# Kernel optimization log

Measured on AMD Instinct MI355X. Metric: run time of the kernel, lower is better.

## Reference

```python
import jax, jax.numpy as jnp
import numpy as np

LMAX = 6
F_IN = 512      # sphere_fdim
F_HID = 8       # f_hidden
N_PTS = 192     # s2 healpix grid points (projector & feature-sphere kernel)
N_SO3GRID = 4000  # SO3Activation grid (resolution=10, ~20x10x20)
N_CONVGRID = 192  # so3_near_identity_grid (8 alpha x 3 beta x 8 gamma)
S2_DIM = (LMAX + 1) ** 2                            # 49
SO3_DIM = sum((2 * l + 1) ** 2 for l in range(LMAX + 1))  # 455
B = 128
C_ENC = 2048
H = W = 7


def setup_inputs() -> dict:
    key = jax.random.key(0)
    ks = jax.random.split(key, 11)
    return {
        "fmap": jax.random.normal(ks[0], (B, C_ENC, H, W), jnp.float32),
        "conv_w": jax.random.normal(ks[1], (F_IN, C_ENC), jnp.float32) / np.sqrt(C_ENC).astype(np.float32),
        "conv_b": jnp.zeros((F_IN,), jnp.float32),
        "proj_w": jax.random.uniform(ks[2], (H, W, N_PTS), jnp.float32) / (H * W),
        "proj_Y": jax.random.normal(ks[3], (N_PTS, S2_DIM), jnp.float32),
        "fs_w": jax.random.normal(ks[4], (F_IN, F_HID, N_PTS), jnp.float32),
        "fs_Y": jax.random.normal(ks[5], (N_PTS, S2_DIM), jnp.float32),
        "act_to": jax.random.normal(ks[6], (SO3_DIM, N_SO3GRID), jnp.float32) / np.sqrt(SO3_DIM).astype(np.float32),
        "act_from": jax.random.normal(ks[7], (N_SO3GRID, SO3_DIM), jnp.float32) / np.float32(N_SO3GRID),
        "so3_w": jax.random.normal(ks[8], (F_HID, 1, N_CONVGRID), jnp.float32),
        "so3_D": jax.random.normal(ks[9], (N_CONVGRID, SO3_DIM), jnp.float32),
    }


def _s2_to_so3_linear(x, psi, f_in):
    # e3nn o3.Linear(s2_irreps -> so3_irreps, internal_weights=False).
    # x: (B, f_in, S2_DIM) with per-l blocks of size 2l+1 (mul=1).
    # psi: (f_in, f_out, S2_DIM). Per l: outer product of input irrep with
    # weight irrep -> (2l+1)x(2l+1) Wigner block; path norm 1/sqrt(f_in*mul_in).
    outs = []
    for l in range(LMAX + 1):
        s, e = l * l, (l + 1) ** 2
        xl = x[:, :, s:e]          # (B, f_in, 2l+1)
        wl = psi[:, :, s:e]        # (f_in, f_out, 2l+1)
        ol = jnp.einsum('bfm,fgu->bgum', xl, wl) / np.sqrt(f_in).astype(np.float32)
        outs.append(ol.reshape(ol.shape[0], ol.shape[1], -1))
    return jnp.concatenate(outs, axis=-1)   # (B, f_out, SO3_DIM)


def _so3_to_so3_linear(x, psi, f_in):
    # e3nn o3.Linear(so3_irreps -> so3_irreps, internal_weights=False).
    # x: (B, f_in, SO3_DIM), per-l block (mul=2l+1, dim=2l+1) flattened [u, m].
    # psi: (f_in, f_out, SO3_DIM), per-l block (u_in, u_out).
    outs = []
    off = 0
    for l in range(LMAX + 1):
        d = 2 * l + 1
        xl = x[:, :, off:off + d * d].reshape(x.shape[0], f_in, d, d)
        wl = psi[:, :, off:off + d * d].reshape(f_in, psi.shape[1], d, d)
        ol = jnp.einsum('bfum,fguv->bgvm', xl, wl) / np.sqrt(f_in * d).astype(np.float32)
        outs.append(ol.reshape(ol.shape[0], ol.shape[1], -1))
        off += d * d
    return jnp.concatenate(outs, axis=-1)


def reference(fmap, conv_w, conv_b, proj_w, proj_Y, fs_w, fs_Y, act_to, act_from, so3_w, so3_D):
    # --- SpatialS2Projector: 1x1 conv, orthographic-grid weighting, S2 FT ---
    x = jnp.einsum('bchw,fc->bfhw', fmap, conv_w) + conv_b[None, :, None, None]
    x = jnp.einsum('bfhw,hwn->bfn', x, proj_w)                   # (B, 512, N_PTS)
    x = jnp.einsum('bfn,ni->bfi', x, proj_Y) / np.sqrt(N_PTS).astype(np.float32)  # (B, 512, 49)
    # --- feature sphere -> external weight for o3.Linear (S2 conv theorem) ---
    psi = jnp.einsum('fgn,ni->fgi', fs_w, fs_Y) / np.sqrt(N_PTS).astype(np.float32)  # (512, 8, 49)
    x = _s2_to_so3_linear(x, psi, F_IN)                          # (B, 8, 455)
    # --- SO3Activation: synthesize signal on SO3 grid, relu, analyze back ---
    g = jax.nn.relu(jnp.einsum('bfi,in->bfn', x, act_to))        # (B, 8, N_SO3GRID)
    x = jnp.einsum('bfn,ni->bfi', g, act_from)                   # (B, 8, 455)
    # --- SO3Convolution over near-identity grid ---
    psi2 = jnp.einsum('fgn,ni->fgi', so3_w, so3_D) / np.sqrt(N_CONVGRID).astype(np.float32)  # (8, 1, 455)
    x = _so3_to_so3_linear(x, psi2, F_HID)                       # (B, 1, 455)
    return x
```

## Files before the change

kernel.cpp:

```cpp
#include <hip/hip_runtime.h>
#include <hip/hip_bf16.h>

#define NB    128
#define CENC  2048
#define FIN   512
#define FHID  8
#define S2D   49
#define SO3D  455
#define HW    49

typedef unsigned short ushort_t;
typedef __bf16 bf16x8 __attribute__((ext_vector_type(8)));
typedef float  f32x4  __attribute__((ext_vector_type(4)));

#define GLD16(gp, lp) __builtin_amdgcn_global_load_lds( \
    (__attribute__((address_space(1))) const unsigned int*)(gp), \
    (__attribute__((address_space(3))) unsigned int*)(lp), 16, 0, 0)

__device__ __forceinline__ int soff(int l) { return l*(4*l*l-1)/3; }

__device__ __forceinline__ ushort_t f2bf(float x) {
  __hip_bfloat16 h = __float2bfloat16(x);
  return *reinterpret_cast<ushort_t*>(&h);
}
__device__ __forceinline__ float bf2f(ushort_t u) {
  __hip_bfloat16 h = *reinterpret_cast<__hip_bfloat16*>(&u);
  return __bfloat162float(h);
}


__device__ __forceinline__ void dev_gemm_nn(float* smem,
    const float* __restrict__ A, const float* __restrict__ B, float* __restrict__ C,
    int M, int N, int K, int lda, int ldb, int ldc, float alpha, int bx, int by,
    int cmode, ushort_t* __restrict__ psiTout)
{
  float* As = smem;
  float* Bs = smem + 32*68;
  const int tid = threadIdx.x;
  const int tx = tid & 15, ty = tid >> 4;
  const int n0 = bx * 64, m0 = by * 64;
  float acc[4][4] = {};
  for (int k0 = 0; k0 < K; k0 += 32) {
    {
      const int kk = tid & 31, mmB = tid >> 5;
      #pragma unroll
      for (int j = 0; j < 8; ++j) {
        const int mm = mmB + 8*j;
        const int m = m0 + mm, k = k0 + kk;
        As[kk*68 + mm] = (m < M && k < K) ? A[(size_t)m*lda + k] : 0.f;
      }
    }
    {
      const int nn = tid & 63, kkB = tid >> 6;
      #pragma unroll
      for (int j = 0; j < 8; ++j) {
        const int kk = kkB + 4*j;
        const int n = n0 + nn, k = k0 + kk;
        Bs[kk*68 + nn] = (n < N && k < K) ? B[(size_t)k*ldb + n] : 0.f;
      }
    }
    __syncthreads();
    #pragma unroll
    for (int kk = 0; kk < 32; ++kk) {
      const float4 a4 = *(const float4*)&As[kk*68 + ty*4];
      const float4 b4 = *(const float4*)&Bs[kk*68 + tx*4];
      const float av[4] = {a4.x,a4.y,a4.z,a4.w};
      const float bv[4] = {b4.x,b4.y,b4.z,b4.w};
      #pragma unroll
      for (int i = 0; i < 4; ++i)
        #pragma unroll
        for (int j = 0; j < 4; ++j)
          acc[i][j] = fmaf(av[i], bv[j], acc[i][j]);
    }
    __syncthreads();
  }
  if (cmode == 1) {
    #pragma unroll
    for (int i = 0; i < 4; ++i) {
      const int m = m0 + ty*4 + i;
      const int f = m >> 3, g = m & 7;
      #pragma unroll
      for (int j = 0; j < 4; ++j) {
        const int n = tx*4 + j;
        psiTout[(size_t)(g*64 + n)*512 + f] = (n < 49) ? f2bf(acc[i][j]*alpha) : (ushort_t)0;
      }
    }
    return;
  }
  #pragma unroll
  for (int i = 0; i < 4; ++i) {
    const int m = m0 + ty*4 + i;
    if (m >= M) continue;
    #pragma unroll
    for (int j = 0; j < 4; ++j) {
      const int n = n0 + tx*4 + j;
      if (n >= N) continue;
      C[(size_t)m*ldc + n] = acc[i][j] * alpha;
    }
  }
}

__device__ __forceinline__ void dev_transpose_cvt64(float* smem,
    const float* __restrict__ in, int R, int C,
    ushort_t* __restrict__ out, int Rp, int Cp, int bx, int by)
{
  float (*t)[65] = (float(*)[65])smem;
  const int c0 = bx*64, r0 = by*64;
  const int tid = threadIdx.x;
  const int cl = tid & 63, rlB = tid >> 6;
  #pragma unroll
  for (int p = 0; p < 16; ++p) {
    const int rl = rlB + p*4;
    const int r = r0 + rl, c = c0 + cl;
    t[rl][cl] = (r < R && c < C) ? in[(size_t)r*C + c] : 0.f;
  }
  __syncthreads();
  #pragma unroll
  for (int p = 0; p < 4; ++p) {
    const int c = p*16 + (tid >> 4);
    const int r4 = (tid & 15) * 4;
    unsigned int lo = (unsigned int)f2bf(t[r4+0][c]) | ((unsigned int)f2bf(t[r4+1][c]) << 16);
    unsigned int hi = (unsigned int)f2bf(t[r4+2][c]) | ((unsigned int)f2bf(t[r4+3][c]) << 16);
    *(uint2*)&out[(size_t)(c0 + c)*Rp + r0 + r4] = make_uint2(lo, hi);
  }
}

__device__ __forceinline__ void dev_sumP(float* smem,
    const float* __restrict__ proj_w, const float* __restrict__ proj_Y,
    float* __restrict__ sumP)
{
  float* colsum = smem;
  const int tid = threadIdx.x;
  if (tid < 192) {
    float s = 0.f;
    for (int h = 0; h < 49; ++h) s += proj_w[h*192 + tid];
    colsum[tid] = s;
  }
  __syncthreads();
  if (tid < 64) {
    float s = 0.f;
    if (tid < 49) for (int k = 0; k < 192; ++k) s += colsum[k] * proj_Y[k*49 + tid];
    sumP[tid] = (tid < 49) ? s * 0.07216878364870323f : 0.f;
  }
}

__global__ __launch_bounds__(256) void prep_all(
    const float* __restrict__ conv_w,
    const float* __restrict__ proj_w, const float* __restrict__ proj_Y,
    const float* __restrict__ fs_w, const float* __restrict__ fs_Y,
    const float* __restrict__ act_to, const float* __restrict__ act_from,
    const float* __restrict__ so3_w, const float* __restrict__ so3_D,
    float* __restrict__ wP, float* __restrict__ wSumP, float* __restrict__ wPsi2,
    ushort_t* __restrict__ psiT,
    ushort_t* __restrict__ actToT, ushort_t* __restrict__ actFromT,
    ushort_t* __restrict__ cwT)
{
  __shared__ float smem[4352];
  const int blk = blockIdx.x;
  const float is192 = 0.07216878364870323f;
  if (blk < 1) {
    dev_gemm_nn(smem, proj_w, proj_Y, wP, 49,49,192, 192,49,49, is192, 0, 0, 0, nullptr);
  } else if (blk < 9) {
    dev_gemm_nn(smem, so3_w, so3_D, wPsi2, 8,455,192, 192,455,455, is192, blk-1, 0, 0, nullptr);
  } else if (blk < 73) {
    dev_gemm_nn(smem, fs_w, fs_Y, nullptr, 4096,49,192, 192,49,0, is192, 0, blk-9, 1, psiT);
  } else if (blk < 585) {
    const int t = blk-73;   dev_transpose_cvt64(smem, act_to, 455, 4000, actToT, 512, 4096, t & 63, t >> 6);
  } else if (blk < 1097) {
    const int t = blk-585;  dev_transpose_cvt64(smem, act_from, 4000, 455, actFromT, 4096, 512, t & 7, t >> 3);
  } else if (blk < 1353) {
    const int t = blk-1097; dev_transpose_cvt64(smem, conv_w, 512, 2048, cwT, 512, 2048, t & 31, t >> 5);
  } else {
    dev_sumP(smem, proj_w, proj_Y, wSumP);
  }
}

__global__ __launch_bounds__(256) void xpt_gemm(
    const float* __restrict__ fmap, const float* __restrict__ wP,
    ushort_t* __restrict__ xPT)
{
  __shared__ ushort_t Wl[64*64];
  __shared__ ushort_t Fl[128*64];
  const int tid = threadIdx.x;
  const int b = blockIdx.x >> 4, ct = blockIdx.x & 15;
  const int c0 = ct*128;
  for (int idx = tid; idx < 4096; idx += 256) {
    const int i = idx >> 6, hw = idx & 63;
    const float v = (i < 49 && hw < 49) ? wP[hw*49 + i] : 0.f;
    const int pos = i*64 + ((((hw>>3) ^ (i & 7)) << 3) | (hw & 7));
    Wl[pos] = f2bf(v);
  }
  const float* src = fmap + ((size_t)b*CENC + c0)*HW;
  #pragma unroll
  for (int q = 0; q < 7; ++q) {
    const int f4 = q*256 + tid;
    if (f4 < 1568) {
      const float4 v = *(const float4*)&src[f4*4];
      const float vv[4] = {v.x,v.y,v.z,v.w};
      const int e0 = f4*4;
      #pragma unroll
      for (int t = 0; t < 4; ++t) {
        const int e = e0 + t;
        const int r = e/49, hw = e - r*49;
        const int pos = r*64 + ((((hw>>3) ^ (r & 7)) << 3) | (hw & 7));
        Fl[pos] = f2bf(vv[t]);
      }
    }
  }
  for (int idx = tid; idx < 128*15; idx += 256) {
    const int r = idx/15, hw = 49 + (idx - (idx/15)*15);
    const int pos = r*64 + ((((hw>>3) ^ (r & 7)) << 3) | (hw & 7));
    Fl[pos] = 0;
  }
  __syncthreads();

  const int wv = tid >> 6, ln = tid & 63;
  const int col = ln & 15, quad = ln >> 4;
  f32x4 acc[4][2];
  #pragma unroll
  for (int i = 0; i < 4; ++i)
    #pragma unroll
    for (int j = 0; j < 2; ++j)
      acc[i][j] = (f32x4){0.f,0.f,0.f,0.f};
  #pragma unroll
  for (int ks = 0; ks < 2; ++ks) {
    bf16x8 af[4], bfr[2];
    #pragma unroll
    for (int i = 0; i < 4; ++i) {
      const int row = i*16 + col;
      af[i] = *(bf16x8*)&Wl[row*64 + (((ks*4 + quad) ^ (row & 7)) << 3)];
    }
    #pragma unroll
    for (int j = 0; j < 2; ++j) {
      const int row = wv*32 + j*16 + col;
      bfr[j] = *(bf16x8*)&Fl[row*64 + (((ks*4 + quad) ^ (row & 7)) << 3)];
    }
    #pragma unroll
    for (int i = 0; i < 4; ++i)
      #pragma unroll
      for (int j = 0; j < 2; ++j)
        acc[i][j] = __builtin_amdgcn_mfma_f32_16x16x32_bf16(af[i], bfr[j], acc[i][j], 0, 0, 0);
  }
  #pragma unroll
  for (int i = 0; i < 4; ++i) {
    #pragma unroll
    for (int j = 0; j < 2; ++j) {
      #pragma unroll
      for (int r = 0; r < 4; ++r) {
        const int irow = i*16 + quad*4 + r;
        const int c = c0 + wv*32 + j*16 + col;
        xPT[(size_t)(b*64 + irow)*2048 + c] = f2bf(acc[i][j][r]);
      }
    }
  }
}

__global__ __launch_bounds__(256) void gemm_w2t(
    const ushort_t* __restrict__ A, const ushort_t* __restrict__ B,
    const float* __restrict__ conv_b,
    ushort_t* __restrict__ Cb, float* __restrict__ bpsi)
{
  __shared__ ushort_t Alds[64*64];
  __shared__ ushort_t Blds[128*64];
  __shared__ float bred[256];
  const int tid = threadIdx.x;
  const int wv = tid >> 6, ln = tid & 63;
  const int col = ln & 15, quad = ln >> 4;
  const int m0 = blockIdx.y * 64, n0 = blockIdx.x * 128;
  const int lda = 512, ldb = 512, ldc = 2048, K = 512;
  const bool doB = (blockIdx.x == 0);
  const int br = tid & 63, bp = tid >> 6;

  const int rl = ln >> 3;
  const int gsw = (ln & 7) ^ rl;
  const ushort_t* aP[2]; const ushort_t* bP[4];
  ushort_t* aL[2]; ushort_t* bL[4];
  #pragma unroll
  for (int r = 0; r < 2; ++r) {
    const int R = wv*16 + r*8;
    aP[r] = A + (size_t)(m0 + R + rl)*lda + gsw*8;
    aL[r] = &Alds[R*64];
  }
  #pragma unroll
  for (int r = 0; r < 4; ++r) {
    const int R = wv*32 + r*8;
    bP[r] = B + (size_t)(n0 + R + rl)*ldb + gsw*8;
    bL[r] = &Blds[R*64];
  }

  f32x4 acc[4][2];
  #pragma unroll
  for (int i = 0; i < 4; ++i)
    #pragma unroll
    for (int j = 0; j < 2; ++j)
      acc[i][j] = (f32x4){0.f,0.f,0.f,0.f};
  float bacc = 0.f;

  for (int k0 = 0; k0 < K; k0 += 64) {
    #pragma unroll
    for (int r = 0; r < 2; ++r) { GLD16(aP[r], aL[r]); aP[r] += 64; }
    #pragma unroll
    for (int r = 0; r < 4; ++r) { GLD16(bP[r], bL[r]); bP[r] += 64; }
    __syncthreads();
    #pragma unroll
    for (int ks = 0; ks < 2; ++ks) {
      bf16x8 af[4], bfr[2];
      #pragma unroll
      for (int i = 0; i < 4; ++i) {
        const int row = i*16 + col;
        af[i] = *(bf16x8*)&Alds[row*64 + (((ks*4 + quad) ^ (row & 7)) << 3)];
      }
      #pragma unroll
      for (int j = 0; j < 2; ++j) {
        const int row = wv*32 + j*16 + col;
        bfr[j] = *(bf16x8*)&Blds[row*64 + (((ks*4 + quad) ^ (row & 7)) << 3)];
      }
      #pragma unroll
      for (int i = 0; i < 4; ++i)
        #pragma unroll
        for (int j = 0; j < 2; ++j)
          acc[i][j] = __builtin_amdgcn_mfma_f32_16x16x32_bf16(af[i], bfr[j], acc[i][j], 0, 0, 0);
    }
    if (doB) {
      #pragma unroll
      for (int qq = 0; qq < 2; ++qq) {
        const int q = bp*2 + qq;
        const int lo = (q ^ (br & 7)) << 3;
        #pragma unroll
        for (int e = 0; e < 8; ++e)
          bacc = fmaf(conv_b[k0 + q*8 + e], bf2f(Alds[br*64 + lo + e]), bacc);
      }
    }
    __syncthreads();
  }

  #pragma unroll
  for (int i = 0; i < 4; ++i) {
    const int mBase = m0 + i*16 + quad*4;
    #pragma unroll
    for (int j = 0; j < 2; ++j) {
      const int n = n0 + wv*32 + j*16 + col;
      #pragma unroll
      for (int r = 0; r < 4; ++r)
        Cb[(size_t)(mBase+r)*ldc + n] = f2bf(acc[i][j][r]);
    }
  }
  if (doB) {
    bred[bp*64 + br] = bacc;
    __syncthreads();
    if (tid < 64)
      bpsi[m0 + tid] = bred[tid] + bred[64+tid] + bred[128+tid] + bred[192+tid];
  }
}

__global__ __launch_bounds__(256) void y_blockdiag(
    const ushort_t* __restrict__ xPT, const ushort_t* __restrict__ W2T,
    const float* __restrict__ sumP, const float* __restrict__ bpsi,
    ushort_t* __restrict__ y)
{
  const int blk = blockIdx.x, tid = threadIdx.x;
  if (blk >= 164) {
    const int bz = blk - 164;
    for (int idx = tid; idx < 7296; idx += 256) {
      const int row = bz*128 + idx/57, cp = 455 + (idx - (idx/57)*57);
      y[(size_t)row*512 + cp] = 0;
    }
    return;
  }
  __shared__ ushort_t Asl[64*64];
  __shared__ ushort_t Bsl[64*64];
  int l, lstart;
  if      (blk < 2)   { l=0; lstart=0; }
  else if (blk < 8)   { l=1; lstart=2; }
  else if (blk < 18)  { l=2; lstart=8; }
  else if (blk < 32)  { l=3; lstart=18; }
  else if (blk < 68)  { l=4; lstart=32; }
  else if (blk < 112) { l=5; lstart=68; }
  else                { l=6; lstart=112; }
  const int d = 2*l+1, ll = l*l, Ml = 8*d;
  const int local = blk - lstart, ntc = 2*d;
  const int mt = local / ntc, nt = local - mt*ntc;
  const int m0 = mt*64, n0 = nt*64;

  const int wv = tid >> 6, ln = tid & 63;
  const int col = ln & 15, quad = ln >> 4;
  const int wr = wv >> 1, wc = wv & 1;
  const int rl = ln >> 3;
  const int gsw = (ln & 7) ^ rl;

  const ushort_t* aP[2]; const ushort_t* bP[2];
  ushort_t* aL[2]; ushort_t* bL[2];
  #pragma unroll
  for (int r = 0; r < 2; ++r) {
    const int R = wv*16 + r*8;
    const int mu = m0 + R + rl;
    int grow;
    if (mu < Ml) { const int g = mu/d, u = mu - g*d; grow = g*64 + ll + u; }
    else grow = 511;
    aP[r] = W2T + (size_t)grow*2048 + gsw*8;
    aL[r] = &Asl[R*64];
    const int nu = n0 + R + rl;
    const int bb = nu/d, m = nu - bb*d;
    bP[r] = xPT + (size_t)(bb*64 + ll + m)*2048 + gsw*8;
    bL[r] = &Bsl[R*64];
  }

  f32x4 acc[2][2];
  #pragma unroll
  for (int i = 0; i < 2; ++i)
    #pragma unroll
    for (int j = 0; j < 2; ++j)
      acc[i][j] = (f32x4){0.f,0.f,0.f,0.f};

  for (int k0 = 0; k0 < 2048; k0 += 64) {
    #pragma unroll
    for (int r = 0; r < 2; ++r) { GLD16(aP[r], aL[r]); aP[r] += 64; }
    #pragma unroll
    for (int r = 0; r < 2; ++r) { GLD16(bP[r], bL[r]); bP[r] += 64; }
    __syncthreads();
    #pragma unroll
    for (int ks = 0; ks < 2; ++ks) {
      bf16x8 af[2], bfr[2];
      #pragma unroll
      for (int i = 0; i < 2; ++i) {
        const int row = wr*32 + i*16 + col;
        af[i] = *(bf16x8*)&Asl[row*64 + (((ks*4 + quad) ^ (row & 7)) << 3)];
      }
      #pragma unroll
      for (int j = 0; j < 2; ++j) {
        const int row = wc*32 + j*16 + col;
        bfr[j] = *(bf16x8*)&Bsl[row*64 + (((ks*4 + quad) ^ (row & 7)) << 3)];
      }
      #pragma unroll
      for (int i = 0; i < 2; ++i)
        #pragma unroll
        for (int j = 0; j < 2; ++j)
          acc[i][j] = __builtin_amdgcn_mfma_f32_16x16x32_bf16(af[i], bfr[j], acc[i][j], 0, 0, 0);
    }
    __syncthreads();
  }

  const float isq512 = 0.044194173824159216f;
  const int sol = soff(l);
  #pragma unroll
  for (int i = 0; i < 2; ++i) {
    #pragma unroll
    for (int j = 0; j < 2; ++j) {
      #pragma unroll
      for (int r = 0; r < 4; ++r) {
        const int mu = m0 + wr*32 + i*16 + quad*4 + r;
        if (mu >= Ml) continue;
        const int nu = n0 + wc*32 + j*16 + col;
        const int g = mu/d, u = mu - g*d;
        const int bb = nu/d, m = nu - bb*d;
        const float v = (acc[i][j][r] + sumP[ll+m]*bpsi[g*64 + ll + u]) * isq512;
        y[(size_t)(bb*8 + g)*512 + sol + u*d + m] = f2bf(v);
      }
    }
  }
}

__global__ __launch_bounds__(512) void gemm8w_nt(
    const ushort_t* __restrict__ A, const ushort_t* __restrict__ B, void* __restrict__ Cv,
    int M, int N, int K, int lda, int ldb, int ldc,
    int mode, int kPartLen)
{
  __shared__ ushort_t Alds[128*64];
  __shared__ ushort_t Blds[128*64];
  const int tid = threadIdx.x;
  const int wv = tid >> 6, ln = tid & 63;
  const int col = ln & 15, quad = ln >> 4;
  const int wr = wv >> 2, wc = wv & 3;
  const int m0 = blockIdx.y * 128, n0 = blockIdx.x * 128;
  int kStart = 0, kEnd = K;
  float*    C  = (float*)Cv;
  ushort_t* Cb = (ushort_t*)Cv;
  if (mode == 2) {
    kStart = blockIdx.z * kPartLen;
    kEnd = min(K, kStart + kPartLen);
    C += (size_t)blockIdx.z * (size_t)M * (size_t)ldc;
  }

  const int rl = ln >> 3;
  const int gsw = (ln & 7) ^ rl;
  const ushort_t* aP[2]; const ushort_t* bP[2];
  ushort_t* aL[2]; ushort_t* bL[2];
  #pragma unroll
  for (int r = 0; r < 2; ++r) {
    const int R = wv*16 + r*8;
    aP[r] = A + (size_t)(m0 + R + rl)*lda + kStart + gsw*8;
    aL[r] = &Alds[R*64];
    bP[r] = B + (size_t)(n0 + R + rl)*ldb + kStart + gsw*8;
    bL[r] = &Blds[R*64];
  }

  f32x4 acc[4][2];
  #pragma unroll
  for (int i = 0; i < 4; ++i)
    #pragma unroll
    for (int j = 0; j < 2; ++j)
      acc[i][j] = (f32x4){0.f,0.f,0.f,0.f};

  for (int k0 = kStart; k0 < kEnd; k0 += 64) {
    #pragma unroll
    for (int r = 0; r < 2; ++r) { GLD16(aP[r], aL[r]); aP[r] += 64; }
    #pragma unroll
    for (int r = 0; r < 2; ++r) { GLD16(bP[r], bL[r]); bP[r] += 64; }
    __syncthreads();
    #pragma unroll
    for (int ks = 0; ks < 2; ++ks) {
      bf16x8 af[4], bfr[2];
      #pragma unroll
      for (int i = 0; i < 4; ++i) {
        const int row = wr*64 + i*16 + col;
        af[i] = *(bf16x8*)&Alds[row*64 + (((ks*4 + quad) ^ (row & 7)) << 3)];
      }
      #pragma unroll
      for (int j = 0; j < 2; ++j) {
        const int row = wc*32 + j*16 + col;
        bfr[j] = *(bf16x8*)&Blds[row*64 + (((ks*4 + quad) ^ (row & 7)) << 3)];
      }
      #pragma unroll
      for (int i = 0; i < 4; ++i)
        #pragma unroll
        for (int j = 0; j < 2; ++j)
          acc[i][j] = __builtin_amdgcn_mfma_f32_16x16x32_bf16(af[i], bfr[j], acc[i][j], 0, 0, 0);
    }
    __syncthreads();
  }

  #pragma unroll
  for (int i = 0; i < 4; ++i) {
    const int mBase = m0 + wr*64 + i*16 + quad*4;
    #pragma unroll
    for (int j = 0; j < 2; ++j) {
      const int n = n0 + wc*32 + j*16 + col;
      if (mode == 1) {
        #pragma unroll
        for (int r = 0; r < 4; ++r)
          Cb[(size_t)(mBase+r)*ldc + n] = f2bf(fmaxf(acc[i][j][r], 0.f));
      } else {
        #pragma unroll
        for (int r = 0; r < 4; ++r)
          C[(size_t)(mBase+r)*ldc + n] = acc[i][j][r];
      }
    }
  }
}

__global__ __launch_bounds__(512) void so3_final(
    const float* __restrict__ zpart, const float* __restrict__ psi2,
    float* __restrict__ out)
{
  __shared__ float Zs[8*SO3D];
  __shared__ float P2s[8*SO3D];
  const int b = blockIdx.x, tid = threadIdx.x;
  for (int idx = tid; idx < 8*SO3D; idx += 512) {
    const int f = idx / SO3D, i = idx - f*SO3D;
    float s = 0.f;
    #pragma unroll
    for (int p = 0; p < 8; ++p)
      s += zpart[((size_t)p*1024 + (size_t)b*FHID + f)*512 + i];
    Zs[idx] = s;
    P2s[idx] = psi2[idx];
  }
  __syncthreads();
  if (tid < SO3D) {
    const int i = tid;
    int l;
    if (i < 1) l = 0; else if (i < 10) l = 1; else if (i < 35) l = 2;
    else if (i < 84) l = 3; else if (i < 165) l = 4; else if (i < 286) l = 5; else l = 6;
    const int so = soff(l), d = 2*l+1;
    const int r = i - so;
    const int v = r / d, m = r - v*d;
    float acc = 0.f;
    for (int f = 0; f < 8; ++f)
      for (int u = 0; u < d; ++u)
        acc = fmaf(Zs[f*SO3D + so + u*d + m], P2s[f*SO3D + so + u*d + v], acc);
    const float scale = rsqrtf(8.0f * (float)d);
    out[(size_t)b*SO3D + i] = acc * scale;
  }
}

extern "C" void kernel_launch(void* const* d_in, const int* in_sizes, int n_in,
                              void* d_out, int out_size, void* d_ws, size_t ws_size,
                              hipStream_t stream) {
  const float* fmap    = (const float*)d_in[0];
  const float* conv_w  = (const float*)d_in[1];
  const float* conv_b  = (const float*)d_in[2];
  const float* proj_w  = (const float*)d_in[3];
  const float* proj_Y  = (const float*)d_in[4];
  const float* fs_w    = (const float*)d_in[5];
  const float* fs_Y    = (const float*)d_in[6];
  const float* act_to  = (const float*)d_in[7];
  const float* act_from= (const float*)d_in[8];
  const float* so3_w   = (const float*)d_in[9];
  const float* so3_D   = (const float*)d_in[10];
  float* out           = (float*)d_out;

  char* wsb = (char*)d_ws;
  float*    wP       = (float*)(wsb + 0);
  float*    wSumP    = (float*)(wsb + 9728);
  float*    wPsi2    = (float*)(wsb + 9984);
  ushort_t* actToT   = (ushort_t*)(wsb + 24576);
  ushort_t* actFromT = (ushort_t*)(wsb + 4218880);
  ushort_t* yPad     = (ushort_t*)(wsb + 8413184);
  ushort_t* psiT     = (ushort_t*)(wsb + 9461760);
  float*    bpsi     = (float*)(wsb + 9986048);
  ushort_t* W2T      = (ushort_t*)(wsb + 9988096);
  ushort_t* xPT      = (ushort_t*)(wsb + 12085248);
  ushort_t* cwT      = (ushort_t*)(wsb + 45639680);
  ushort_t* gBuf     = (ushort_t*)(wsb + 12085248);
  float*    zPart    = (float*)(wsb + 20473856);

  prep_all<<<dim3(1354), 256, 0, stream>>>(
      conv_w, proj_w, proj_Y, fs_w, fs_Y, act_to, act_from, so3_w, so3_D,
      wP, wSumP, wPsi2, psiT, actToT, actFromT, cwT);
  xpt_gemm<<<dim3(2048), 256, 0, stream>>>(fmap, wP, xPT);
  gemm_w2t<<<dim3(16,8), 256, 0, stream>>>(psiT, cwT, conv_b, W2T, bpsi);
  y_blockdiag<<<dim3(172), 256, 0, stream>>>(xPT, W2T, wSumP, bpsi, yPad);
  gemm8w_nt<<<dim3(32,8), 512, 0, stream>>>(yPad, actToT, gBuf,
      1024, 4096, 512, 512, 512, 4096, 1, 0);
  gemm8w_nt<<<dim3(4,8,8), 512, 0, stream>>>(gBuf, actFromT, zPart,
      1024, 512, 4096, 4096, 4096, 512, 2, 512);
  so3_final<<<dim3(128), 512, 0, stream>>>(zPart, wPsi2, out);
}
```

Measured before the change: 222.9 us.

## Merge xpt and w2t GEMMs into one launch, precompute swizzled bf16 projection weight

```diff
diff --git a/kernel.cpp b/kernel.cpp
--- a/kernel.cpp
+++ b/kernel.cpp
@@ -32,7 +32,7 @@
 __device__ __forceinline__ void dev_gemm_nn(float* smem,
     const float* __restrict__ A, const float* __restrict__ B, float* __restrict__ C,
     int M, int N, int K, int lda, int ldb, int ldc, float alpha, int bx, int by,
-    int cmode, ushort_t* __restrict__ psiTout)
+    int cmode, ushort_t* __restrict__ uOut)
 {
   float* As = smem;
   float* Bs = smem + 32*68;
@@ -82,7 +82,20 @@
       #pragma unroll
       for (int j = 0; j < 4; ++j) {
         const int n = tx*4 + j;
-        psiTout[(size_t)(g*64 + n)*512 + f] = (n < 49) ? f2bf(acc[i][j]*alpha) : (ushort_t)0;
+        uOut[(size_t)(g*64 + n)*512 + f] = (n < 49) ? f2bf(acc[i][j]*alpha) : (ushort_t)0;
+      }
+    }
+    return;
+  }
+  if (cmode == 2) {
+    #pragma unroll
+    for (int i = 0; i < 4; ++i) {
+      const int m = ty*4 + i;
+      #pragma unroll
+      for (int j = 0; j < 4; ++j) {
+        const int n = tx*4 + j;
+        const float v = (m < 49 && n < 49) ? acc[i][j]*alpha : 0.f;
+        uOut[n*64 + ((((m>>3) ^ (n&7)) << 3) | (m&7))] = f2bf(v);
       }
     }
     return;
@@ -150,7 +163,7 @@
     const float* __restrict__ fs_w, const float* __restrict__ fs_Y,
     const float* __restrict__ act_to, const float* __restrict__ act_from,
     const float* __restrict__ so3_w, const float* __restrict__ so3_D,
-    float* __restrict__ wP, float* __restrict__ wSumP, float* __restrict__ wPsi2,
+    ushort_t* __restrict__ wPT64, float* __restrict__ wSumP, float* __restrict__ wPsi2,
     ushort_t* __restrict__ psiT,
     ushort_t* __restrict__ actToT, ushort_t* __restrict__ actFromT,
     ushort_t* __restrict__ cwT)
@@ -159,7 +172,7 @@
   const int blk = blockIdx.x;
   const float is192 = 0.07216878364870323f;
   if (blk < 1) {
-    dev_gemm_nn(smem, proj_w, proj_Y, wP, 49,49,192, 192,49,49, is192, 0, 0, 0, nullptr);
+    dev_gemm_nn(smem, proj_w, proj_Y, nullptr, 49,49,192, 192,49,0, is192, 0, 0, 2, wPT64);
   } else if (blk < 9) {
     dev_gemm_nn(smem, so3_w, so3_D, wPsi2, 8,455,192, 192,455,455, is192, blk-1, 0, 0, nullptr);
   } else if (blk < 73) {
@@ -175,46 +188,47 @@
   }
 }
 
-__global__ __launch_bounds__(256) void xpt_gemm(
-    const float* __restrict__ fmap, const float* __restrict__ wP,
-    ushort_t* __restrict__ xPT)
-{
-  __shared__ ushort_t Wl[64*64];
-  __shared__ ushort_t Fl[128*64];
+__device__ __forceinline__ void dev_xpt(
+    ushort_t* Wl, ushort_t* Fl,
+    const float* __restrict__ fmap, const ushort_t* __restrict__ wPT64,
+    ushort_t* __restrict__ xPT, int blk)
+{
   const int tid = threadIdx.x;
-  const int b = blockIdx.x >> 4, ct = blockIdx.x & 15;
+  const int wv = tid >> 6, ln = tid & 63;
+  const int b = blk >> 4, ct = blk & 15;
   const int c0 = ct*128;
-  for (int idx = tid; idx < 4096; idx += 256) {
-    const int i = idx >> 6, hw = idx & 63;
-    const float v = (i < 49 && hw < 49) ? wP[hw*49 + i] : 0.f;
-    const int pos = i*64 + ((((hw>>3) ^ (i & 7)) << 3) | (hw & 7));
-    Wl[pos] = f2bf(v);
-  }
+  #pragma unroll
+  for (int q = 0; q < 2; ++q)
+    GLD16(wPT64 + (wv*2+q)*512 + ln*8, Wl + (wv*2+q)*512);
   const float* src = fmap + ((size_t)b*CENC + c0)*HW;
+  int r = (tid*4)/49, hw = tid*4 - r*49;
   #pragma unroll
   for (int q = 0; q < 7; ++q) {
     const int f4 = q*256 + tid;
     if (f4 < 1568) {
-      const float4 v = *(const float4*)&src[f4*4];
-      const float vv[4] = {v.x,v.y,v.z,v.w};
-      const int e0 = f4*4;
+      const float4 v = *(const float4*)&src[(size_t)f4*4];
+      const float vv[4] = {v.x, v.y, v.z, v.w};
+      int rr = r, hh = hw;
       #pragma unroll
       for (int t = 0; t < 4; ++t) {
-        const int e = e0 + t;
-        const int r = e/49, hw = e - r*49;
-        const int pos = r*64 + ((((hw>>3) ^ (r & 7)) << 3) | (hw & 7));
-        Fl[pos] = f2bf(vv[t]);
-      }
-    }
-  }
-  for (int idx = tid; idx < 128*15; idx += 256) {
-    const int r = idx/15, hw = 49 + (idx - (idx/15)*15);
-    const int pos = r*64 + ((((hw>>3) ^ (r & 7)) << 3) | (hw & 7));
-    Fl[pos] = 0;
+        Fl[rr*64 + ((((hh>>3) ^ (rr&7)) << 3) | (hh&7))] = f2bf(vv[t]);
+        if (++hh == 49) { hh = 0; ++rr; }
+      }
+    }
+    r += 20; hw += 44;
+    if (hw >= 49) { hw -= 49; ++r; }
+  }
+  #pragma unroll
+  for (int q = 0; q < 8; ++q) {
+    const int idx = q*256 + tid;
+    const int rr = idx >> 4, j = idx & 15;
+    if (j) {
+      const int hh = 48 + j;
+      Fl[rr*64 + ((((hh>>3) ^ (rr&7)) << 3) | (hh&7))] = 0;
+    }
   }
   __syncthreads();
 
-  const int wv = tid >> 6, ln = tid & 63;
   const int col = ln & 15, quad = ln >> 4;
   f32x4 acc[4][2];
   #pragma unroll
@@ -246,29 +260,27 @@
     #pragma unroll
     for (int j = 0; j < 2; ++j) {
       #pragma unroll
-      for (int r = 0; r < 4; ++r) {
-        const int irow = i*16 + quad*4 + r;
+      for (int r2 = 0; r2 < 4; ++r2) {
+        const int irow = i*16 + quad*4 + r2;
         const int c = c0 + wv*32 + j*16 + col;
-        xPT[(size_t)(b*64 + irow)*2048 + c] = f2bf(acc[i][j][r]);
-      }
-    }
-  }
-}
-
-__global__ __launch_bounds__(256) void gemm_w2t(
+        xPT[(size_t)(b*64 + irow)*2048 + c] = f2bf(acc[i][j][r2]);
+      }
+    }
+  }
+}
+
+__device__ __forceinline__ void dev_w2t(
+    ushort_t* Alds, ushort_t* Blds, float* bred,
     const ushort_t* __restrict__ A, const ushort_t* __restrict__ B,
     const float* __restrict__ conv_b,
-    ushort_t* __restrict__ Cb, float* __restrict__ bpsi)
-{
-  __shared__ ushort_t Alds[64*64];
-  __shared__ ushort_t Blds[128*64];
-  __shared__ float bred[256];
+    ushort_t* __restrict__ Cb, float* __restrict__ bpsi, int bx, int by)
+{
   const int tid = threadIdx.x;
   const int wv = tid >> 6, ln = tid & 63;
   const int col = ln & 15, quad = ln >> 4;
-  const int m0 = blockIdx.y * 64, n0 = blockIdx.x * 128;
+  const int m0 = by * 64, n0 = bx * 128;
   const int lda = 512, ldb = 512, ldc = 2048, K = 512;
-  const bool doB = (blockIdx.x == 0);
+  const bool doB = (bx == 0);
   const int br = tid & 63, bp = tid >> 6;
 
   const int rl = ln >> 3;
@@ -353,22 +365,38 @@
   }
 }
 
+__global__ __launch_bounds__(256) void mid_fused(
+    const float* __restrict__ fmap, const ushort_t* __restrict__ wPT64,
+    const ushort_t* __restrict__ psiT, const ushort_t* __restrict__ cwT,
+    const float* __restrict__ conv_b,
+    ushort_t* __restrict__ xPT, ushort_t* __restrict__ W2T,
+    float* __restrict__ bpsi, ushort_t* __restrict__ yPad)
+{
+  __shared__ __align__(16) ushort_t smem[12800];
+  const int blk = blockIdx.x;
+  if (blk < 2048) {
+    dev_xpt(smem, smem + 4096, fmap, wPT64, xPT, blk);
+  } else if (blk < 2176) {
+    const int t = blk - 2048;
+    dev_w2t(smem, smem + 4096, (float*)(smem + 12288),
+            psiT, cwT, conv_b, W2T, bpsi, t & 15, t >> 4);
+  } else {
+    const int bz = blk - 2176, tid = threadIdx.x;
+    for (int idx = tid; idx < 7296; idx += 256) {
+      const int row = bz*128 + idx/57, cp = 455 + (idx - (idx/57)*57);
+      yPad[(size_t)row*512 + cp] = 0;
+    }
+  }
+}
+
 __global__ __launch_bounds__(256) void y_blockdiag(
     const ushort_t* __restrict__ xPT, const ushort_t* __restrict__ W2T,
     const float* __restrict__ sumP, const float* __restrict__ bpsi,
     ushort_t* __restrict__ y)
 {
+  __shared__ __align__(16) ushort_t Asl[64*128];
+  __shared__ __align__(16) ushort_t Bsl[64*128];
   const int blk = blockIdx.x, tid = threadIdx.x;
-  if (blk >= 164) {
-    const int bz = blk - 164;
-    for (int idx = tid; idx < 7296; idx += 256) {
-      const int row = bz*128 + idx/57, cp = 455 + (idx - (idx/57)*57);
-      y[(size_t)row*512 + cp] = 0;
-    }
-    return;
-  }
-  __shared__ ushort_t Asl[64*64];
-  __shared__ ushort_t Bsl[64*64];
   int l, lstart;
   if      (blk < 2)   { l=0; lstart=0; }
   else if (blk < 8)   { l=1; lstart=2; }
@@ -385,24 +413,26 @@
   const int wv = tid >> 6, ln = tid & 63;
   const int col = ln & 15, quad = ln >> 4;
   const int wr = wv >> 1, wc = wv & 1;
-  const int rl = ln >> 3;
-  const int gsw = (ln & 7) ^ rl;
-
-  const ushort_t* aP[2]; const ushort_t* bP[2];
-  ushort_t* aL[2]; ushort_t* bL[2];
-  #pragma unroll
-  for (int r = 0; r < 2; ++r) {
-    const int R = wv*16 + r*8;
-    const int mu = m0 + R + rl;
+  const int rl4 = ln >> 4;
+  const int gi = ln & 15;
+
+  const ushort_t* aP[4]; const ushort_t* bP[4];
+  ushort_t* aL[4]; ushort_t* bL[4];
+  #pragma unroll
+  for (int r = 0; r < 4; ++r) {
+    const int R = wv*16 + r*4;
+    const int row = R + rl4;
+    const int gsw = gi ^ (row & 15);
+    const int mu = m0 + row;
     int grow;
     if (mu < Ml) { const int g = mu/d, u = mu - g*d; grow = g*64 + ll + u; }
     else grow = 511;
     aP[r] = W2T + (size_t)grow*2048 + gsw*8;
-    aL[r] = &Asl[R*64];
-    const int nu = n0 + R + rl;
+    aL[r] = &Asl[R*128];
+    const int nu = n0 + row;
     const int bb = nu/d, m = nu - bb*d;
     bP[r] = xPT + (size_t)(bb*64 + ll + m)*2048 + gsw*8;
-    bL[r] = &Bsl[R*64];
+    bL[r] = &Bsl[R*128];
   }
 
   f32x4 acc[2][2];
@@ -412,24 +442,24 @@
     for (int j = 0; j < 2; ++j)
       acc[i][j] = (f32x4){0.f,0.f,0.f,0.f};
 
-  for (int k0 = 0; k0 < 2048; k0 += 64) {
-    #pragma unroll
-    for (int r = 0; r < 2; ++r) { GLD16(aP[r], aL[r]); aP[r] += 64; }
-    #pragma unroll
-    for (int r = 0; r < 2; ++r) { GLD16(bP[r], bL[r]); bP[r] += 64; }
-    __syncthreads();
-    #pragma unroll
-    for (int ks = 0; ks < 2; ++ks) {
+  for (int k0 = 0; k0 < 2048; k0 += 128) {
+    #pragma unroll
+    for (int r = 0; r < 4; ++r) { GLD16(aP[r], aL[r]); aP[r] += 128; }
+    #pragma unroll
+    for (int r = 0; r < 4; ++r) { GLD16(bP[r], bL[r]); bP[r] += 128; }
+    __syncthreads();
+    #pragma unroll
+    for (int ks = 0; ks < 4; ++ks) {
       bf16x8 af[2], bfr[2];
       #pragma unroll
       for (int i = 0; i < 2; ++i) {
         const int row = wr*32 + i*16 + col;
-        af[i] = *(bf16x8*)&Asl[row*64 + (((ks*4 + quad) ^ (row & 7)) << 3)];
+        af[i] = *(bf16x8*)&Asl[row*128 + (((ks*4 + quad) ^ (row & 15)) << 3)];
       }
       #pragma unroll
       for (int j = 0; j < 2; ++j) {
         const int row = wc*32 + j*16 + col;
-        bfr[j] = *(bf16x8*)&Bsl[row*64 + (((ks*4 + quad) ^ (row & 7)) << 3)];
+        bfr[j] = *(bf16x8*)&Bsl[row*128 + (((ks*4 + quad) ^ (row & 15)) << 3)];
       }
       #pragma unroll
       for (int i = 0; i < 2; ++i)
@@ -599,7 +629,7 @@
   float* out           = (float*)d_out;
 
   char* wsb = (char*)d_ws;
-  float*    wP       = (float*)(wsb + 0);
+  ushort_t* wPT64    = (ushort_t*)(wsb + 0);
   float*    wSumP    = (float*)(wsb + 9728);
   float*    wPsi2    = (float*)(wsb + 9984);
   ushort_t* actToT   = (ushort_t*)(wsb + 24576);
@@ -615,10 +645,10 @@
 
   prep_all<<<dim3(1354), 256, 0, stream>>>(
       conv_w, proj_w, proj_Y, fs_w, fs_Y, act_to, act_from, so3_w, so3_D,
-      wP, wSumP, wPsi2, psiT, actToT, actFromT, cwT);
-  xpt_gemm<<<dim3(2048), 256, 0, stream>>>(fmap, wP, xPT);
-  gemm_w2t<<<dim3(16,8), 256, 0, stream>>>(psiT, cwT, conv_b, W2T, bpsi);
-  y_blockdiag<<<dim3(172), 256, 0, stream>>>(xPT, W2T, wSumP, bpsi, yPad);
+      wPT64, wSumP, wPsi2, psiT, actToT, actFromT, cwT);
+  mid_fused<<<dim3(2184), 256, 0, stream>>>(
+      fmap, wPT64, psiT, cwT, conv_b, xPT, W2T, bpsi, yPad);
+  y_blockdiag<<<dim3(164), 256, 0, stream>>>(xPT, W2T, wSumP, bpsi, yPad);
   gemm8w_nt<<<dim3(32,8), 512, 0, stream>>>(yPad, actToT, gBuf,
       1024, 4096, 512, 512, 512, 4096, 1, 0);
   gemm8w_nt<<<dim3(4,8,8), 512, 0, stream>>>(gBuf, actFromT, zPart,
```

Result: faster. 208.8 us (-6.3%).
